# Performance work log

Hardware: AMD Instinct MI355X
Metric: run time of the kernel (lower is better)

Reference implementation:

```python
import jax, jax.numpy as jnp
import numpy as np

B = 256
H = W = 14
HW = H * W
TS = 0.03  # sigmoid temperature
TC = 0.07  # contrastive temperature
TP_K = int(HW * 0.1)   # 19
TN_K = int(HW * 0.5)   # 98
EPS_NORM = 1e-12
EPS_PD = 1e-6  # torch F.pairwise_distance eps


def _l2norm(x, axis):
    n = jnp.sqrt(jnp.sum(x * x, axis=axis, keepdims=True))
    return x / jnp.maximum(n, EPS_NORM)


def _conv(x, w):
    return jax.lax.conv_general_dilated(
        x, w, window_strides=(1, 1), padding='SAME',
        dimension_numbers=('NCHW', 'OIHW', 'NCHW'))


def setup_inputs() -> dict:
    key = jax.random.key(0)
    ks = jax.random.split(key, 7)
    ev = jax.random.normal(ks[0], (B, 384, H, W), dtype=jnp.float32)
    ea = jax.random.normal(ks[1], (B, 2048), dtype=jnp.float32)
    masks = jax.random.randint(ks[2], (B, H, W), 0, 2).astype(jnp.int32)
    masks = masks.at[:, 0, 0].set(1)  # guarantee nonzero mask area
    W_fc1 = jax.random.normal(ks[3], (512, 2048), dtype=jnp.float32) * 0.02
    W_fc2 = jax.random.normal(ks[4], (512, 512), dtype=jnp.float32) * 0.02
    W_conv1 = jax.random.normal(ks[5], (512, 384, 3, 3), dtype=jnp.float32) * 0.02
    W_conv2 = jax.random.normal(ks[6], (512, 512, 3, 3), dtype=jnp.float32) * 0.02
    return {'ev': ev, 'ea': ea, 'masks': masks, 'W_fc1': W_fc1,
            'W_fc2': W_fc2, 'W_conv1': W_conv1, 'W_conv2': W_conv2}


def reference(ev, ea, masks, W_fc1, W_fc2, W_conv1, W_conv2):
    # Audio_Proj: fc2(relu(fc1(ea)))  -> (B, 512)
    fa = jnp.maximum(ea @ W_fc1.T, 0.0) @ W_fc2.T

    # Visual_Proj: conv2(relu(conv1(ev))) -> (B, 512, 14, 14)
    fv_map = _conv(jnp.maximum(_conv(ev, W_conv1), 0.0), W_conv2)
    fv_map_norm = _l2norm(fv_map, axis=1)

    # masked mean pooling over the Ncut mask -> indicator vector (B, 512)
    m = masks.astype(jnp.float32)
    ind_vec = jnp.sum(fv_map * m[:, None], axis=(2, 3)) / jnp.sum(m, axis=(1, 2))[:, None]
    ind_vec_norm = _l2norm(ind_vec, axis=1)

    # Sij[i, j, p] = <fv_map_norm[i, :, p], ind_vec_norm[j]>  -> (B, B, HW)
    Sij = jnp.einsum('ichw,jc->ijhw', fv_map_norm, ind_vec_norm).reshape(B, B, HW)

    # per-row topk thresholds (kth largest / kth smallest)
    pos_thr = jax.lax.top_k(Sij, TP_K)[0][..., -1:]           # (B, B, 1)
    neg_thr = -jax.lax.top_k(-Sij, TN_K)[0][..., -1:]         # (B, B, 1)

    m_p = jax.nn.sigmoid((Sij - pos_thr) / TS)
    m_n = 1.0 - jax.nn.sigmoid((Sij - neg_thr) / TS)

    SP = jnp.sum(Sij * m_p, axis=-1) / jnp.sum(m_p, axis=-1)  # (B, B)
    SN = jnp.sum(Sij * m_n, axis=-1) / jnp.sum(m_n, axis=-1)  # (B, B)

    logits1 = jnp.concatenate([SP, SN], axis=1) / TC          # (B, 2B)
    logits2 = jnp.concatenate([SP.T, SN.T], axis=1) / TC
    labels = jnp.arange(B)
    loss1 = -jnp.mean(jax.nn.log_softmax(logits1, axis=-1)[labels, labels])
    loss2 = -jnp.mean(jax.nn.log_softmax(logits2, axis=-1)[labels, labels])

    # squared pairwise distance between detached ind_vec and fa (torch eps in diff)
    diff = jax.lax.stop_gradient(ind_vec)[:, None, :] - fa[None, :, :] + EPS_PD
    dist_mat = jnp.sum(diff * diff, axis=-1)                  # (B, B)

    ivn_d = jax.lax.stop_gradient(ind_vec_norm)
    vv_logits = ivn_d @ ivn_d.T
    eye = jnp.eye(B, dtype=jnp.float32)
    w = -vv_logits * (1.0 - eye) + eye
    dist_mat = dist_mat * w

    mask_mat = eye - (1.0 - eye) / (B - 1)
    loss3 = jnp.mean(jnp.maximum(jnp.sum(dist_mat * mask_mat, axis=1) + 0.6, 0.0))
    loss4 = jnp.mean(jnp.maximum(jnp.sum(dist_mat * mask_mat, axis=0) + 0.6, 0.0))

    return ((loss1 + loss2) / 2.0, (loss3 + loss4) / 2.0)
```

## Files before the change

### kernel.cpp

```cpp
#include <hip/hip_runtime.h>
#include <stdint.h>


typedef __attribute__((ext_vector_type(8))) short bf16x8;
typedef __attribute__((ext_vector_type(4))) short short4v;
typedef __attribute__((ext_vector_type(4))) float f32x4;

__device__ __forceinline__ unsigned short f2bf(float x) {
  unsigned u = __float_as_uint(x);
  unsigned r = u + 0x7FFFu + ((u >> 16) & 1u);
  return (unsigned short)(r >> 16);
}
__device__ __forceinline__ float bf2f(unsigned short h) {
  return __uint_as_float(((unsigned)h) << 16);
}

typedef const __attribute__((address_space(1))) void* gptr1_t;
typedef __attribute__((address_space(3))) void* lptr3_t;
__device__ __forceinline__ void gload_lds16(const void* g, void* l) {
  __builtin_amdgcn_global_load_lds((gptr1_t)g, (lptr3_t)l, 16, 0, 0);
}

__device__ __forceinline__ float waveSum(float v) {
#pragma unroll
  for (int m = 1; m < 64; m <<= 1) v += __shfl_xor(v, m, 64);
  return v;
}
__device__ __forceinline__ float waveMax(float v) {
#pragma unroll
  for (int m = 1; m < 64; m <<= 1) v = fmaxf(v, __shfl_xor(v, m, 64));
  return v;
}
template <int NW>
__device__ __forceinline__ float blockSum(float v) {
  __shared__ float sh[NW];
  v = waveSum(v);
  int wv = threadIdx.x >> 6, ln = threadIdx.x & 63;
  if (ln == 0) sh[wv] = v;
  __syncthreads();
  float r = 0.f;
#pragma unroll
  for (int w = 0; w < NW; ++w) r += sh[w];
  __syncthreads();
  return r;
}
template <int NW>
__device__ __forceinline__ float blockMax(float v) {
  __shared__ float sh[NW];
  v = waveMax(v);
  int wv = threadIdx.x >> 6, ln = threadIdx.x & 63;
  if (ln == 0) sh[wv] = v;
  __syncthreads();
  float r = -3.4e38f;
#pragma unroll
  for (int w = 0; w < NW; ++w) r = fmaxf(r, sh[w]);
  __syncthreads();
  return r;
}

#define RA 65536

template <int KC, int EPI>
__global__ __launch_bounds__(256, 2) void convtap6_k(
    const unsigned short* __restrict__ A, const unsigned short* __restrict__ Bw,
    unsigned short* __restrict__ C) {
  __shared__ __align__(16) short Ah[256 * 72];
  const int tid = threadIdx.x;
  const int wave = tid >> 6, lane = tid & 63;
  const int wm = wave >> 1, wn = wave & 1;
  const int quad = lane >> 4, tq = lane & 15;
  const int img = blockIdx.x, n0 = blockIdx.y * 128;

  int pab[7];
  {
    const int dh = tq >> 3;
    int wq = wm * 8 + (tq & 7);
    if (wq == 0) wq = 8;
    else if (wq == 15) wq = 7;
#pragma unroll
    for (int mi = 0; mi < 7; ++mi) {
      int pr = (1 + 2 * mi + dh) * 16 + wq;
      pab[mi] = (pr - 17) * 144 + quad * 16;
    }
  }
  const int gb = (n0 >> 4) + wn * 4;

  const char* Ab = (const char*)A;
  const char* AhB = (const char*)Ah;
  const int l16 = lane * 16;

  f32x4 acc[7][4];
#pragma unroll
  for (int mi = 0; mi < 7; ++mi)
#pragma unroll
    for (int ni = 0; ni < 4; ++ni) {
      f32x4 z = {0.f, 0.f, 0.f, 0.f};
      acc[mi][ni] = z;
    }

  auto stageA = [&](int kc) {
    size_t s0 = ((size_t)kc * RA + img * 256) * 144;
#pragma unroll
    for (int i = 0; i < 9; ++i) {
      int c = wave + i * 4;
      gload_lds16(Ab + s0 + (size_t)c * 1024 + l16, (char*)Ah + c * 1024);
    }
  };

  stageA(0);
  bf16x8 b0[4], b1[4];
  {
    const size_t w0 = ((size_t)gb * 128 + lane) * 8;
#pragma unroll
    for (int ni = 0; ni < 4; ++ni)
      b0[ni] = *(const bf16x8*)&Bw[w0 + (size_t)ni * 1024];
  }
  __syncthreads();

#pragma unroll 1
  for (int kc = 0; kc < KC; ++kc) {
    const size_t bk = ((size_t)kc * 4096 + gb * 128 + lane) * 8;
#pragma unroll
    for (int t = 0; t < 9; ++t) {
      const size_t tof = (size_t)t * KC * 32768;
#pragma unroll
      for (int ni = 0; ni < 4; ++ni)
        b1[ni] = *(const bf16x8*)&Bw[bk + tof + (size_t)ni * 1024 + 512];
      bf16x8 b0n[4];
      const bool last = (t == 8) && (kc == KC - 1);
      if (!last) {
        const size_t nbase =
            (t < 8) ? bk + (size_t)(t + 1) * KC * 32768 : bk + 32768;
#pragma unroll
        for (int ni = 0; ni < 4; ++ni)
          b0n[ni] = *(const bf16x8*)&Bw[nbase + (size_t)ni * 1024];
      }
      const int OFF = (17 + (t / 3 - 1) * 16 + (t % 3 - 1)) * 144;
      bf16x8 af0[7], af1[7];
#pragma unroll
      for (int mi = 0; mi < 7; ++mi)
        af0[mi] = *(const bf16x8*)(AhB + pab[mi] + OFF);
#pragma unroll
      for (int mi = 0; mi < 7; ++mi)
        af1[mi] = *(const bf16x8*)(AhB + pab[mi] + OFF + 64);
      __builtin_amdgcn_s_setprio(1);
#pragma unroll
      for (int mi = 0; mi < 7; ++mi)
#pragma unroll
        for (int ni = 0; ni < 4; ++ni)
          acc[mi][ni] = __builtin_amdgcn_mfma_f32_16x16x32_bf16(
              af0[mi], b0[ni], acc[mi][ni], 0, 0, 0);
#pragma unroll
      for (int mi = 0; mi < 7; ++mi)
#pragma unroll
        for (int ni = 0; ni < 4; ++ni)
          acc[mi][ni] = __builtin_amdgcn_mfma_f32_16x16x32_bf16(
              af1[mi], b1[ni], acc[mi][ni], 0, 0, 0);
      __builtin_amdgcn_s_setprio(0);
      if (!last) {
#pragma unroll
        for (int ni = 0; ni < 4; ++ni) b0[ni] = b0n[ni];
      }
    }
    if (kc + 1 < KC) {
      __syncthreads();
      stageA(kc + 1);
      __syncthreads();
    }
  }

#pragma unroll
  for (int mi = 0; mi < 7; ++mi) {
#pragma unroll
    for (int r = 0; r < 4; ++r) {
      int idx = quad * 4 + r;
      int wv = wm * 8 + (idx & 7);
      if (wv == 0 || wv == 15) continue;
      int hh = 1 + 2 * mi + (idx >> 3);
      short4v s4;
#pragma unroll
      for (int ni = 0; ni < 4; ++ni) {
        float v = acc[mi][ni][r];
        s4[ni] = (short)f2bf(EPI == 0 ? fmaxf(v, 0.f) : v);
      }
      if (EPI == 0) {
        int cell = img * 256 + hh * 16 + wv;
        int slice = (n0 >> 6) + wn;
        size_t ob = ((size_t)slice * RA + cell) * 72 + tq * 4;
        *(short4v*)&C[ob] = s4;
      } else {
        int p = (hh - 1) * 14 + (wv - 1);
        size_t ob = (size_t)(img * 196 + p) * 512 + n0 + wn * 64 + tq * 4;
        *(short4v*)&C[ob] = s4;
      }
    }
  }
}

template <int K, int NLD, int EPI>
__global__ __launch_bounds__(256, 2) void gemm1_k(
    const unsigned short* __restrict__ A, const unsigned short* __restrict__ Bw,
    void* __restrict__ C, const float* __restrict__ rs) {
  __shared__ short As[128 * 64];
  __shared__ short Bs[128 * 64];
  const int tid = threadIdx.x;
  const int wave = tid >> 6, lane = tid & 63;
  const int m0 = blockIdx.x * 128, n0 = blockIdx.y * 128;
  const int rr8 = lane >> 3, seg = lane & 7, gseg = seg ^ rr8;
  const int wm = wave >> 1, wn = wave & 1;
  const int quad = lane >> 4, tq = lane & 15;

  size_t asrc[4], bsrc[4];
#pragma unroll
  for (int i8 = 0; i8 < 4; ++i8) {
    int rloc = wave * 32 + i8 * 8 + rr8;
    asrc[i8] = (size_t)(m0 + rloc) * K + gseg * 8;
    bsrc[i8] = (size_t)(n0 + rloc) * K + gseg * 8;
  }

  f32x4 acc[4][4];
#pragma unroll
  for (int mi = 0; mi < 4; ++mi)
#pragma unroll
    for (int ni = 0; ni < 4; ++ni) {
      f32x4 z = {0.f, 0.f, 0.f, 0.f};
      acc[mi][ni] = z;
    }

#pragma unroll 1
  for (int kc2 = 0; kc2 < K / 64; ++kc2) {
    int kb = kc2 * 64;
    __syncthreads();
#pragma unroll
    for (int i8 = 0; i8 < 4; ++i8) {
      gload_lds16(A + asrc[i8] + kb, &As[(wave * 32 + i8 * 8) * 64]);
      gload_lds16(Bw + bsrc[i8] + kb, &Bs[(wave * 32 + i8 * 8) * 64]);
    }
    __syncthreads();
#pragma unroll
    for (int h = 0; h < 2; ++h) {
      bf16x8 af[4], bfr[4];
#pragma unroll
      for (int mi = 0; mi < 4; ++mi) {
        int row = wm * 64 + mi * 16 + tq;
        af[mi] = *(const bf16x8*)&As[row * 64 +
                                     ((((h << 2) | quad) ^ (row & 7)) << 3)];
      }
#pragma unroll
      for (int ni = 0; ni < 4; ++ni) {
        int row = wn * 64 + ni * 16 + tq;
        bfr[ni] = *(const bf16x8*)&Bs[row * 64 +
                                      ((((h << 2) | quad) ^ (row & 7)) << 3)];
      }
#pragma unroll
      for (int mi = 0; mi < 4; ++mi)
#pragma unroll
        for (int ni = 0; ni < 4; ++ni)
          acc[mi][ni] = __builtin_amdgcn_mfma_f32_16x16x32_bf16(
              af[mi], bfr[ni], acc[mi][ni], 0, 0, 0);
    }
  }

#pragma unroll
  for (int mi = 0; mi < 4; ++mi) {
#pragma unroll
    for (int r = 0; r < 4; ++r) {
      int m = m0 + wm * 64 + mi * 16 + quad * 4 + r;
      float sc = (EPI == 3) ? rs[m] : 1.f;
      size_t obase = (size_t)m * NLD + n0 + wn * 64 + tq;
#pragma unroll
      for (int ni = 0; ni < 4; ++ni) {
        float v = acc[mi][ni][r];
        size_t idx = obase + ni * 16;
        if (EPI == 0)
          ((unsigned short*)C)[idx] = f2bf(fmaxf(v, 0.f));
        else if (EPI == 2)
          ((float*)C)[idx] = v;
        else
          ((float*)C)[idx] = v * sc;
      }
    }
  }
}

__global__ __launch_bounds__(256, 2) void gemm_xv_k(
    const unsigned short* __restrict__ ivpb, const unsigned short* __restrict__ fab,
    const unsigned short* __restrict__ indnb, float* __restrict__ Xm,
    float* __restrict__ Vm) {
  const unsigned short* A = blockIdx.z ? indnb : ivpb;
  const unsigned short* Bw = blockIdx.z ? indnb : fab;
  float* C = blockIdx.z ? Vm : Xm;
  __shared__ short As[128 * 64];
  __shared__ short Bs[128 * 64];
  const int tid = threadIdx.x;
  const int wave = tid >> 6, lane = tid & 63;
  const int m0 = blockIdx.x * 128, n0 = blockIdx.y * 128;
  const int rr8 = lane >> 3, seg = lane & 7, gseg = seg ^ rr8;
  const int wm = wave >> 1, wn = wave & 1;
  const int quad = lane >> 4, tq = lane & 15;
  size_t asrc[4], bsrc[4];
#pragma unroll
  for (int i8 = 0; i8 < 4; ++i8) {
    int rloc = wave * 32 + i8 * 8 + rr8;
    asrc[i8] = (size_t)(m0 + rloc) * 512 + gseg * 8;
    bsrc[i8] = (size_t)(n0 + rloc) * 512 + gseg * 8;
  }
  f32x4 acc[4][4];
#pragma unroll
  for (int mi = 0; mi < 4; ++mi)
#pragma unroll
    for (int ni = 0; ni < 4; ++ni) {
      f32x4 z = {0.f, 0.f, 0.f, 0.f};
      acc[mi][ni] = z;
    }
#pragma unroll 1
  for (int kc2 = 0; kc2 < 8; ++kc2) {
    int kb = kc2 * 64;
    __syncthreads();
#pragma unroll
    for (int i8 = 0; i8 < 4; ++i8) {
      gload_lds16(A + asrc[i8] + kb, &As[(wave * 32 + i8 * 8) * 64]);
      gload_lds16(Bw + bsrc[i8] + kb, &Bs[(wave * 32 + i8 * 8) * 64]);
    }
    __syncthreads();
#pragma unroll
    for (int h = 0; h < 2; ++h) {
      bf16x8 af[4], bfr[4];
#pragma unroll
      for (int mi = 0; mi < 4; ++mi) {
        int row = wm * 64 + mi * 16 + tq;
        af[mi] = *(const bf16x8*)&As[row * 64 +
                                     ((((h << 2) | quad) ^ (row & 7)) << 3)];
      }
#pragma unroll
      for (int ni = 0; ni < 4; ++ni) {
        int row = wn * 64 + ni * 16 + tq;
        bfr[ni] = *(const bf16x8*)&Bs[row * 64 +
                                      ((((h << 2) | quad) ^ (row & 7)) << 3)];
      }
#pragma unroll
      for (int mi = 0; mi < 4; ++mi)
#pragma unroll
        for (int ni = 0; ni < 4; ++ni)
          acc[mi][ni] = __builtin_amdgcn_mfma_f32_16x16x32_bf16(
              af[mi], bfr[ni], acc[mi][ni], 0, 0, 0);
    }
  }
#pragma unroll
  for (int mi = 0; mi < 4; ++mi)
#pragma unroll
    for (int r = 0; r < 4; ++r) {
      int m = m0 + wm * 64 + mi * 16 + quad * 4 + r;
      size_t obase = (size_t)m * 256 + n0 + wn * 64 + tq;
#pragma unroll
      for (int ni = 0; ni < 4; ++ni) C[obase + ni * 16] = acc[mi][ni][r];
    }
}

__global__ void prep_all_k(const float* __restrict__ ea,
                           const float* __restrict__ Wf1,
                           const float* __restrict__ Wf2,
                           const float* __restrict__ Wc1,
                           const float* __restrict__ Wc2,
                           unsigned short* __restrict__ eab,
                           unsigned short* __restrict__ wf1b,
                           unsigned short* __restrict__ wf2b,
                           unsigned short* __restrict__ wb1,
                           unsigned short* __restrict__ wb2,
                           unsigned int* __restrict__ x1u) {
  int i = blockIdx.x * 256 + threadIdx.x;
  if (i < 524288) {
    eab[i] = f2bf(ea[i]);
  } else if (i < 1572864) {
    int j = i - 524288;
    wf1b[j] = f2bf(Wf1[j]);
  } else if (i < 1835008) {
    int j = i - 1572864;
    wf2b[j] = f2bf(Wf2[j]);
  } else if (i < 3604480) {
    int j = i - 1835008;
    int t = j / (6 * 32768), r = j - t * (6 * 32768);
    int kc = r / 32768, r2 = r - kc * 32768;
    int g = r2 >> 10, h = (r2 >> 9) & 1, quad = (r2 >> 7) & 3;
    int tq = (r2 >> 3) & 15, jj = r2 & 7;
    int n = g * 16 + tq, cin = kc * 64 + h * 32 + quad * 8 + jj;
    wb1[j] = f2bf(Wc1[(n * 384 + cin) * 9 + t]);
  } else if (i < 5963776) {
    int j = i - 3604480;
    int t = j / (8 * 32768), r = j - t * (8 * 32768);
    int kc = r / 32768, r2 = r - kc * 32768;
    int g = r2 >> 10, h = (r2 >> 9) & 1, quad = (r2 >> 7) & 3;
    int tq = (r2 >> 3) & 15, jj = r2 & 7;
    int n = g * 16 + tq;
    int cin = kc * 64 + (jj & 3) * 16 + h * 8 + quad * 2 + (jj >> 2);
    wb2[j] = f2bf(Wc2[(n * 512 + cin) * 9 + t]);
  } else {
    int j = i - 5963776;
    int hr = j >> 8, u = j & 255;
    int slice = u >> 5, uu = u & 31;
    int b = hr / 60, c = hr - b * 60;
    int cell;
    if (c < 16) cell = c;
    else if (c < 32) cell = 240 + (c - 16);
    else if (c < 46) cell = (c - 31) * 16;
    else cell = (c - 45) * 16 + 15;
    x1u[((size_t)slice * RA + b * 256 + cell) * 36 + uu] = 0u;
  }
}

__global__ __launch_bounds__(256) void evpad_k(const float* __restrict__ ev,
                                               unsigned short* __restrict__ out) {
  int b = blockIdx.x, ct = blockIdx.y;
  __shared__ float tile[64][197];
  int tid = threadIdx.x;
  const float* src = ev + ((size_t)b * 384 + ct * 64) * 196;
#pragma unroll 1
  for (int it = 0; it < 49; ++it) {
    int idx = it * 256 + tid;
    int c = idx / 196, p = idx - c * 196;
    tile[c][p] = src[idx];
  }
  __syncthreads();
  unsigned short* dst = out + ((size_t)ct * RA + b * 256) * 72;
#pragma unroll 1
  for (int it = 0; it < 64; ++it) {
    int idx = it * 256 + tid;
    int cell = idx >> 6, c = idx & 63;
    int h = (cell >> 4) - 1, w = (cell & 15) - 1;
    float v = ((unsigned)h < 14u && (unsigned)w < 14u) ? tile[c][h * 14 + w]
                                                       : 0.f;
    dst[(size_t)cell * 72 + c] = f2bf(v);
  }
}


__global__ __launch_bounds__(512) void pool_k(
    const unsigned short* __restrict__ fv, const int* __restrict__ masks,
    unsigned short* __restrict__ indnb, unsigned short* __restrict__ ivpb,
    float* __restrict__ Pi, float* __restrict__ rn) {
  int b = blockIdx.x;
  int w = threadIdx.x >> 6, lane = threadIdx.x & 63;
  __shared__ float red[8][512];
  __shared__ float msh[8];
  float acc[8] = {0.f, 0.f, 0.f, 0.f, 0.f, 0.f, 0.f, 0.f};
  float msum = 0.f;
  for (int p = w; p < 196; p += 8) {
    float m = (float)masks[b * 196 + p];
    msum += m;
    uint4 d = *(const uint4*)(fv + (size_t)(b * 196 + p) * 512 + lane * 8);
    const unsigned short* hp = (const unsigned short*)&d;
    float ss = 0.f;
#pragma unroll
    for (int k = 0; k < 8; ++k) {
      float x = bf2f(hp[k]);
      ss += x * x;
      acc[k] += m * x;
    }
    ss = waveSum(ss);
    if (lane == 0) rn[b * 196 + p] = 1.f / fmaxf(sqrtf(ss), 1e-12f);
  }
#pragma unroll
  for (int k = 0; k < 8; ++k) red[w][lane * 8 + k] = acc[k];
  if (lane == 0) msh[w] = msum;
  __syncthreads();
  int tid = threadIdx.x;
  float s = 0.f, mtot = 0.f;
#pragma unroll
  for (int ww = 0; ww < 8; ++ww) {
    s += red[ww][tid];
    mtot += msh[ww];
  }
  float v = s / mtot;
  float ss2 = blockSum<8>(v * v);
  float sc = 1.f / fmaxf(sqrtf(ss2), 1e-12f);
  indnb[b * 512 + tid] = f2bf(v * sc);
  float ve = v + 1e-6f;
  ivpb[b * 512 + tid] = f2bf(ve);
  float p2 = blockSum<8>(ve * ve);
  if (tid == 0) Pi[b] = p2;
}

__global__ __launch_bounds__(512) void fanorm_k(const float* __restrict__ fa,
                                                unsigned short* __restrict__ fab,
                                                float* __restrict__ Qj) {
  int b = blockIdx.x, tid = threadIdx.x;
  int s64 = tid & 63;
  int chan = (tid & ~63) | ((s64 & 3) * 16 + (s64 >> 2));
  float v = fa[b * 512 + chan];
  fab[b * 512 + tid] = f2bf(v);
  float q = blockSum<8>(v * v);
  if (tid == 0) Qj[b] = q;
}


__device__ __forceinline__ float radix_kth(unsigned k0, unsigned k1, unsigned k2,
                                           unsigned k3, int k) {
  unsigned prefix = 0;
  int kk = k;
#pragma unroll 1
  for (int bit = 31; bit >= 14; --bit) {
    unsigned thi = (prefix >> bit) | 1u;
    int c = __popcll(__ballot((k0 >> bit) == thi)) +
            __popcll(__ballot((k1 >> bit) == thi)) +
            __popcll(__ballot((k2 >> bit) == thi)) +
            __popcll(__ballot((k3 >> bit) == thi));
    if (kk <= c)
      prefix |= (1u << bit);
    else
      kk -= c;
  }
  unsigned u = (prefix & 0x80000000u) ? (prefix ^ 0x80000000u) : ~prefix;
  return __uint_as_float(u);
}
__device__ __forceinline__ unsigned sortkey(float x) {
  unsigned u = __float_as_uint(x);
  return u ^ (((int)u >> 31) | 0x80000000u);
}

__global__ __launch_bounds__(256) void spsn_k(const float* __restrict__ Sij,
                                              float* __restrict__ SP,
                                              float* __restrict__ SN) {
  int i = blockIdx.x, jg = blockIdx.y;
  int tid = threadIdx.x, wave = tid >> 6, lane = tid & 63;
  __shared__ float tile[196 * 65];
#pragma unroll 1
  for (int it = 0; it < 49; ++it) {
    int lin = it * 256 + tid;
    int p = lin >> 6, j = lin & 63;
    tile[p * 65 + j] = Sij[(size_t)(i * 196 + p) * 256 + jg * 64 + j];
  }
  __syncthreads();
#pragma unroll 1
  for (int jj = 0; jj < 16; ++jj) {
    int j = jj * 4 + wave;
    float v0 = tile[lane * 65 + j];
    float v1 = tile[(lane + 64) * 65 + j];
    float v2 = tile[(lane + 128) * 65 + j];
    bool val3 = lane < 4;
    float v3 = val3 ? tile[(lane + 192) * 65 + j] : 0.f;
    unsigned k0 = sortkey(v0), k1 = sortkey(v1), k2 = sortkey(v2);
    unsigned k3 = val3 ? sortkey(v3) : 0u;
    float thrP = radix_kth(k0, k1, k2, k3, 19);
    float thrN = radix_kth(k0, k1, k2, k3, 99);
    float spn = 0.f, spd = 0.f, snn = 0.f, snd = 0.f;
    const float invTS = 1.f / 0.03f;
#pragma unroll
    for (int q = 0; q < 4; ++q) {
      float v = (q == 0) ? v0 : (q == 1) ? v1 : (q == 2) ? v2 : v3;
      bool ok = (q < 3) || val3;
      if (ok) {
        float mp = 1.f / (1.f + __expf((thrP - v) * invTS));
        float mn = 1.f / (1.f + __expf((v - thrN) * invTS));
        spn += v * mp;
        spd += mp;
        snn += v * mn;
        snd += mn;
      }
    }
    spn = waveSum(spn); spd = waveSum(spd);
    snn = waveSum(snn); snd = waveSum(snd);
    if (lane == 0) {
      SP[i * 256 + jg * 64 + j] = spn / spd;
      SN[i * 256 + jg * 64 + j] = snn / snd;
    }
  }
}

__global__ __launch_bounds__(256) void loss12_k(const float* __restrict__ SP,
                                                const float* __restrict__ SN,
                                                float* __restrict__ out) {
  int r = blockIdx.x;
  int i = r & 255;
  bool col = r >= 256;
  int tid = threadIdx.x;
  const float invTC = 1.f / 0.07f;
  float a = (col ? SP[tid * 256 + i] : SP[i * 256 + tid]) * invTC;
  float b = (col ? SN[tid * 256 + i] : SN[i * 256 + tid]) * invTC;
  float mx = blockMax<4>(fmaxf(a, b));
  float se = blockSum<4>(__expf(a - mx) + __expf(b - mx));
  float lse = mx + __logf(se);
  if (tid == 0) {
    float diag = SP[i * 256 + i] * invTC;
    atomicAdd(out, -(diag - lse) * (1.f / 512.f));
  }
}

__global__ __launch_bounds__(256) void distcomb_k(
    const float* __restrict__ Pi, const float* __restrict__ Qj,
    const float* __restrict__ X, const float* __restrict__ V,
    float* __restrict__ val, float* __restrict__ out) {
  int i = blockIdx.x, j = threadIdx.x;
  float d = Pi[i] - 2.f * X[i * 256 + j] + Qj[j];
  float w = (i == j) ? 1.f : -V[i * 256 + j];
  float x = d * w;
  val[i * 256 + j] = x;
  __shared__ float diag_sh;
  if (j == i) diag_sh = x;
  float tot = blockSum<4>(x);
  if (j == 0) {
    float rs = diag_sh - (tot - diag_sh) * (1.f / 255.f);
    atomicAdd(out + 1, fmaxf(rs + 0.6f, 0.f) * (1.f / 512.f));
  }
}

__global__ __launch_bounds__(256) void loss4_k(const float* __restrict__ val,
                                               float* __restrict__ out) {
  int j = blockIdx.x, i = threadIdx.x;
  float x = val[i * 256 + j];
  __shared__ float diag_sh;
  if (i == j) diag_sh = x;
  float tot = blockSum<4>(x);
  if (i == 0) {
    float cs = diag_sh - (tot - diag_sh) * (1.f / 255.f);
    atomicAdd(out + 1, fmaxf(cs + 0.6f, 0.f) * (1.f / 512.f));
  }
}


extern "C" void kernel_launch(void* const* d_in, const int* in_sizes, int n_in,
                              void* d_out, int out_size, void* d_ws,
                              size_t ws_size, hipStream_t stream) {
  (void)in_sizes; (void)n_in; (void)out_size; (void)ws_size;
  const float* ev = (const float*)d_in[0];
  const float* ea = (const float*)d_in[1];
  const int* msk = (const int*)d_in[2];
  const float* Wf1 = (const float*)d_in[3];
  const float* Wf2 = (const float*)d_in[4];
  const float* Wc1 = (const float*)d_in[5];
  const float* Wc2 = (const float*)d_in[6];
  float* out = (float*)d_out;
  char* ws = (char*)d_ws;

  size_t off = 0;
  auto alloc = [&](size_t bytes) {
    void* p = ws + off;
    off = (off + bytes + 255) & ~(size_t)255;
    return p;
  };
  unsigned short* evb = (unsigned short*)alloc((size_t)6 * RA * 144);
  unsigned short* fv = evb;
  unsigned short* x1b = (unsigned short*)alloc((size_t)8 * RA * 144);
  float* Sij = (float*)x1b;
  unsigned short* wb1 = (unsigned short*)alloc((size_t)9 * 6 * 32768 * 2);
  unsigned short* wb2 = (unsigned short*)alloc((size_t)9 * 8 * 32768 * 2);
  unsigned short* eab = (unsigned short*)alloc((size_t)256 * 2048 * 2);
  unsigned short* wf1b = (unsigned short*)alloc((size_t)512 * 2048 * 2);
  unsigned short* wf2b = (unsigned short*)alloc((size_t)512 * 512 * 2);
  unsigned short* hb = (unsigned short*)alloc((size_t)256 * 512 * 2);
  float* fa = (float*)alloc((size_t)256 * 512 * 4);
  unsigned short* indnb = (unsigned short*)alloc((size_t)256 * 512 * 2);
  unsigned short* ivpb = (unsigned short*)alloc((size_t)256 * 512 * 2);
  unsigned short* fab = (unsigned short*)alloc((size_t)256 * 512 * 2);
  float* Pi = (float*)alloc(256 * 4);
  float* Qj = (float*)alloc(256 * 4);
  float* Xm = (float*)alloc((size_t)256 * 256 * 4);
  float* Vm = (float*)alloc((size_t)256 * 256 * 4);
  float* rn = (float*)alloc((size_t)50176 * 4);
  float* SP = (float*)alloc((size_t)256 * 256 * 4);
  float* SN = (float*)alloc((size_t)256 * 256 * 4);
  float* val = (float*)alloc((size_t)256 * 256 * 4);

  hipMemsetAsync(out, 0, 2 * sizeof(float), stream);

  prep_all_k<<<38656, 256, 0, stream>>>(ea, Wf1, Wf2, Wc1, Wc2, eab, wf1b,
                                        wf2b, wb1, wb2, (unsigned int*)x1b);
  evpad_k<<<dim3(256, 6), 256, 0, stream>>>(ev, evb);

  convtap6_k<6, 0><<<dim3(256, 4), 256, 0, stream>>>(evb, wb1, x1b);
  gemm1_k<2048, 512, 0><<<dim3(2, 4), 256, 0, stream>>>(eab, wf1b, hb, nullptr);
  gemm1_k<512, 512, 2><<<dim3(2, 4), 256, 0, stream>>>(hb, wf2b, fa, nullptr);
  convtap6_k<8, 1><<<dim3(256, 4), 256, 0, stream>>>(x1b, wb2, fv);

  pool_k<<<256, 512, 0, stream>>>(fv, msk, indnb, ivpb, Pi, rn);
  fanorm_k<<<256, 512, 0, stream>>>(fa, fab, Qj);

  gemm1_k<512, 256, 3><<<dim3(392, 2), 256, 0, stream>>>(fv, indnb, Sij, rn);
  gemm_xv_k<<<dim3(2, 2, 2), 256, 0, stream>>>(ivpb, fab, indnb, Xm, Vm);

  spsn_k<<<dim3(256, 4), 256, 0, stream>>>(Sij, SP, SN);
  loss12_k<<<512, 256, 0, stream>>>(SP, SN, out);
  distcomb_k<<<256, 256, 0, stream>>>(Pi, Qj, Xm, Vm, val, out);
  loss4_k<<<256, 256, 0, stream>>>(val, out);
}
```

Before: 777.4 us.

## Double-buffer GEMM LDS staging and merge small pool/fa and loss kernels

The two generic GEMM kernels now use two LDS buffers, so the global-to-LDS load of the next K-chunk is issued before the MFMA work on the current chunk, and there is one barrier per iteration instead of two. Separately, pool and fa-normalization are fused into one launch, and the loss12 and distcomb kernels are merged into one launch, to cut launch overhead. Doubling LDS to 64KB per block may reduce occupancy under the launch bound of 2 blocks per CU.

After: 767.8 us, median of 2. About the same (-1.2%).

```diff
diff --git a/kernel.cpp b/kernel.cpp
--- a/kernel.cpp
+++ b/kernel.cpp
@@ -201,8 +201,8 @@
 __global__ __launch_bounds__(256, 2) void gemm1_k(
     const unsigned short* __restrict__ A, const unsigned short* __restrict__ Bw,
     void* __restrict__ C, const float* __restrict__ rs) {
-  __shared__ short As[128 * 64];
-  __shared__ short Bs[128 * 64];
+  __shared__ short As[2][128 * 64];
+  __shared__ short Bs[2][128 * 64];
   const int tid = threadIdx.x;
   const int wave = tid >> 6, lane = tid & 63;
   const int m0 = blockIdx.x * 128, n0 = blockIdx.y * 128;
@@ -218,6 +218,15 @@
     bsrc[i8] = (size_t)(n0 + rloc) * K + gseg * 8;
   }
 
+  auto stage = [&](int kc2, int buf) {
+    int kb = kc2 * 64;
+#pragma unroll
+    for (int i8 = 0; i8 < 4; ++i8) {
+      gload_lds16(A + asrc[i8] + kb, &As[buf][(wave * 32 + i8 * 8) * 64]);
+      gload_lds16(Bw + bsrc[i8] + kb, &Bs[buf][(wave * 32 + i8 * 8) * 64]);
+    }
+  };
+
   f32x4 acc[4][4];
 #pragma unroll
   for (int mi = 0; mi < 4; ++mi)
@@ -227,30 +236,27 @@
       acc[mi][ni] = z;
     }
 
-#pragma unroll 1
-  for (int kc2 = 0; kc2 < K / 64; ++kc2) {
-    int kb = kc2 * 64;
-    __syncthreads();
-#pragma unroll
-    for (int i8 = 0; i8 < 4; ++i8) {
-      gload_lds16(A + asrc[i8] + kb, &As[(wave * 32 + i8 * 8) * 64]);
-      gload_lds16(Bw + bsrc[i8] + kb, &Bs[(wave * 32 + i8 * 8) * 64]);
-    }
-    __syncthreads();
+  const int NK = K / 64;
+  stage(0, 0);
+  __syncthreads();
+#pragma unroll 1
+  for (int kc2 = 0; kc2 < NK; ++kc2) {
+    const int cur = kc2 & 1;
+    if (kc2 + 1 < NK) stage(kc2 + 1, cur ^ 1);
 #pragma unroll
     for (int h = 0; h < 2; ++h) {
       bf16x8 af[4], bfr[4];
 #pragma unroll
       for (int mi = 0; mi < 4; ++mi) {
         int row = wm * 64 + mi * 16 + tq;
-        af[mi] = *(const bf16x8*)&As[row * 64 +
-                                     ((((h << 2) | quad) ^ (row & 7)) << 3)];
+        af[mi] = *(const bf16x8*)&As[cur][row * 64 +
+                                         ((((h << 2) | quad) ^ (row & 7)) << 3)];
       }
 #pragma unroll
       for (int ni = 0; ni < 4; ++ni) {
         int row = wn * 64 + ni * 16 + tq;
-        bfr[ni] = *(const bf16x8*)&Bs[row * 64 +
-                                      ((((h << 2) | quad) ^ (row & 7)) << 3)];
+        bfr[ni] = *(const bf16x8*)&Bs[cur][row * 64 +
+                                           ((((h << 2) | quad) ^ (row & 7)) << 3)];
       }
 #pragma unroll
       for (int mi = 0; mi < 4; ++mi)
@@ -259,6 +265,7 @@
           acc[mi][ni] = __builtin_amdgcn_mfma_f32_16x16x32_bf16(
               af[mi], bfr[ni], acc[mi][ni], 0, 0, 0);
     }
+    __syncthreads();
   }
 
 #pragma unroll
@@ -290,8 +297,8 @@
   const unsigned short* A = blockIdx.z ? indnb : ivpb;
   const unsigned short* Bw = blockIdx.z ? indnb : fab;
   float* C = blockIdx.z ? Vm : Xm;
-  __shared__ short As[128 * 64];
-  __shared__ short Bs[128 * 64];
+  __shared__ short As[2][128 * 64];
+  __shared__ short Bs[2][128 * 64];
   const int tid = threadIdx.x;
   const int wave = tid >> 6, lane = tid & 63;
   const int m0 = blockIdx.x * 128, n0 = blockIdx.y * 128;
@@ -305,6 +312,14 @@
     asrc[i8] = (size_t)(m0 + rloc) * 512 + gseg * 8;
     bsrc[i8] = (size_t)(n0 + rloc) * 512 + gseg * 8;
   }
+  auto stage = [&](int kc2, int buf) {
+    int kb = kc2 * 64;
+#pragma unroll
+    for (int i8 = 0; i8 < 4; ++i8) {
+      gload_lds16(A + asrc[i8] + kb, &As[buf][(wave * 32 + i8 * 8) * 64]);
+      gload_lds16(Bw + bsrc[i8] + kb, &Bs[buf][(wave * 32 + i8 * 8) * 64]);
+    }
+  };
   f32x4 acc[4][4];
 #pragma unroll
   for (int mi = 0; mi < 4; ++mi)
@@ -313,30 +328,26 @@
       f32x4 z = {0.f, 0.f, 0.f, 0.f};
       acc[mi][ni] = z;
     }
+  stage(0, 0);
+  __syncthreads();
 #pragma unroll 1
   for (int kc2 = 0; kc2 < 8; ++kc2) {
-    int kb = kc2 * 64;
-    __syncthreads();
-#pragma unroll
-    for (int i8 = 0; i8 < 4; ++i8) {
-      gload_lds16(A + asrc[i8] + kb, &As[(wave * 32 + i8 * 8) * 64]);
-      gload_lds16(Bw + bsrc[i8] + kb, &Bs[(wave * 32 + i8 * 8) * 64]);
-    }
-    __syncthreads();
+    const int cur = kc2 & 1;
+    if (kc2 + 1 < 8) stage(kc2 + 1, cur ^ 1);
 #pragma unroll
     for (int h = 0; h < 2; ++h) {
       bf16x8 af[4], bfr[4];
 #pragma unroll
       for (int mi = 0; mi < 4; ++mi) {
         int row = wm * 64 + mi * 16 + tq;
-        af[mi] = *(const bf16x8*)&As[row * 64 +
-                                     ((((h << 2) | quad) ^ (row & 7)) << 3)];
+        af[mi] = *(const bf16x8*)&As[cur][row * 64 +
+                                         ((((h << 2) | quad) ^ (row & 7)) << 3)];
       }
 #pragma unroll
       for (int ni = 0; ni < 4; ++ni) {
         int row = wn * 64 + ni * 16 + tq;
-        bfr[ni] = *(const bf16x8*)&Bs[row * 64 +
-                                      ((((h << 2) | quad) ^ (row & 7)) << 3)];
+        bfr[ni] = *(const bf16x8*)&Bs[cur][row * 64 +
+                                           ((((h << 2) | quad) ^ (row & 7)) << 3)];
       }
 #pragma unroll
       for (int mi = 0; mi < 4; ++mi)
@@ -345,6 +356,7 @@
           acc[mi][ni] = __builtin_amdgcn_mfma_f32_16x16x32_bf16(
               af[mi], bfr[ni], acc[mi][ni], 0, 0, 0);
     }
+    __syncthreads();
   }
 #pragma unroll
   for (int mi = 0; mi < 4; ++mi)
@@ -433,13 +445,25 @@
   }
 }
 
-
-__global__ __launch_bounds__(512) void pool_k(
+__global__ __launch_bounds__(512) void poolfa_k(
     const unsigned short* __restrict__ fv, const int* __restrict__ masks,
-    unsigned short* __restrict__ indnb, unsigned short* __restrict__ ivpb,
-    float* __restrict__ Pi, float* __restrict__ rn) {
-  int b = blockIdx.x;
-  int w = threadIdx.x >> 6, lane = threadIdx.x & 63;
+    const float* __restrict__ fa, unsigned short* __restrict__ indnb,
+    unsigned short* __restrict__ ivpb, unsigned short* __restrict__ fab,
+    float* __restrict__ Pi, float* __restrict__ Qj, float* __restrict__ rn) {
+  int bid = blockIdx.x;
+  int tid = threadIdx.x;
+  if (bid >= 256) {
+    int b = bid - 256;
+    int s64 = tid & 63;
+    int chan = (tid & ~63) | ((s64 & 3) * 16 + (s64 >> 2));
+    float v = fa[b * 512 + chan];
+    fab[b * 512 + tid] = f2bf(v);
+    float q = blockSum<8>(v * v);
+    if (tid == 0) Qj[b] = q;
+    return;
+  }
+  int b = bid;
+  int w = tid >> 6, lane = tid & 63;
   __shared__ float red[8][512];
   __shared__ float msh[8];
   float acc[8] = {0.f, 0.f, 0.f, 0.f, 0.f, 0.f, 0.f, 0.f};
@@ -463,7 +487,6 @@
   for (int k = 0; k < 8; ++k) red[w][lane * 8 + k] = acc[k];
   if (lane == 0) msh[w] = msum;
   __syncthreads();
-  int tid = threadIdx.x;
   float s = 0.f, mtot = 0.f;
 #pragma unroll
   for (int ww = 0; ww < 8; ++ww) {
@@ -478,18 +501,6 @@
   ivpb[b * 512 + tid] = f2bf(ve);
   float p2 = blockSum<8>(ve * ve);
   if (tid == 0) Pi[b] = p2;
-}
-
-__global__ __launch_bounds__(512) void fanorm_k(const float* __restrict__ fa,
-                                                unsigned short* __restrict__ fab,
-                                                float* __restrict__ Qj) {
-  int b = blockIdx.x, tid = threadIdx.x;
-  int s64 = tid & 63;
-  int chan = (tid & ~63) | ((s64 & 3) * 16 + (s64 >> 2));
-  float v = fa[b * 512 + chan];
-  fab[b * 512 + tid] = f2bf(v);
-  float q = blockSum<8>(v * v);
-  if (tid == 0) Qj[b] = q;
 }
 
 
@@ -566,40 +577,39 @@
   }
 }
 
-__global__ __launch_bounds__(256) void loss12_k(const float* __restrict__ SP,
-                                                const float* __restrict__ SN,
-                                                float* __restrict__ out) {
-  int r = blockIdx.x;
-  int i = r & 255;
-  bool col = r >= 256;
-  int tid = threadIdx.x;
-  const float invTC = 1.f / 0.07f;
-  float a = (col ? SP[tid * 256 + i] : SP[i * 256 + tid]) * invTC;
-  float b = (col ? SN[tid * 256 + i] : SN[i * 256 + tid]) * invTC;
-  float mx = blockMax<4>(fmaxf(a, b));
-  float se = blockSum<4>(__expf(a - mx) + __expf(b - mx));
-  float lse = mx + __logf(se);
-  if (tid == 0) {
-    float diag = SP[i * 256 + i] * invTC;
-    atomicAdd(out, -(diag - lse) * (1.f / 512.f));
-  }
-}
-
-__global__ __launch_bounds__(256) void distcomb_k(
+__global__ __launch_bounds__(256) void lossA_k(
+    const float* __restrict__ SP, const float* __restrict__ SN,
     const float* __restrict__ Pi, const float* __restrict__ Qj,
     const float* __restrict__ X, const float* __restrict__ V,
     float* __restrict__ val, float* __restrict__ out) {
-  int i = blockIdx.x, j = threadIdx.x;
-  float d = Pi[i] - 2.f * X[i * 256 + j] + Qj[j];
-  float w = (i == j) ? 1.f : -V[i * 256 + j];
-  float x = d * w;
-  val[i * 256 + j] = x;
-  __shared__ float diag_sh;
-  if (j == i) diag_sh = x;
-  float tot = blockSum<4>(x);
-  if (j == 0) {
-    float rs = diag_sh - (tot - diag_sh) * (1.f / 255.f);
-    atomicAdd(out + 1, fmaxf(rs + 0.6f, 0.f) * (1.f / 512.f));
+  int r = blockIdx.x;
+  int tid = threadIdx.x;
+  if (r < 512) {
+    int i = r & 255;
+    bool col = r >= 256;
+    const float invTC = 1.f / 0.07f;
+    float a = (col ? SP[tid * 256 + i] : SP[i * 256 + tid]) * invTC;
+    float b = (col ? SN[tid * 256 + i] : SN[i * 256 + tid]) * invTC;
+    float mx = blockMax<4>(fmaxf(a, b));
+    float se = blockSum<4>(__expf(a - mx) + __expf(b - mx));
+    float lse = mx + __logf(se);
+    if (tid == 0) {
+      float diag = SP[i * 256 + i] * invTC;
+      atomicAdd(out, -(diag - lse) * (1.f / 512.f));
+    }
+  } else {
+    int i = r - 512, j = tid;
+    float d = Pi[i] - 2.f * X[i * 256 + j] + Qj[j];
+    float w = (i == j) ? 1.f : -V[i * 256 + j];
+    float x = d * w;
+    val[i * 256 + j] = x;
+    __shared__ float diag_sh;
+    if (j == i) diag_sh = x;
+    float tot = blockSum<4>(x);
+    if (j == 0) {
+      float rs = diag_sh - (tot - diag_sh) * (1.f / 255.f);
+      atomicAdd(out + 1, fmaxf(rs + 0.6f, 0.f) * (1.f / 512.f));
+    }
   }
 }
 
@@ -671,14 +681,12 @@
   gemm1_k<512, 512, 2><<<dim3(2, 4), 256, 0, stream>>>(hb, wf2b, fa, nullptr);
   convtap6_k<8, 1><<<dim3(256, 4), 256, 0, stream>>>(x1b, wb2, fv);
 
-  pool_k<<<256, 512, 0, stream>>>(fv, msk, indnb, ivpb, Pi, rn);
-  fanorm_k<<<256, 512, 0, stream>>>(fa, fab, Qj);
+  poolfa_k<<<512, 512, 0, stream>>>(fv, msk, fa, indnb, ivpb, fab, Pi, Qj, rn);
 
   gemm1_k<512, 256, 3><<<dim3(392, 2), 256, 0, stream>>>(fv, indnb, Sij, rn);
   gemm_xv_k<<<dim3(2, 2, 2), 256, 0, stream>>>(ivpb, fab, indnb, Xm, Vm);
 
   spsn_k<<<dim3(256, 4), 256, 0, stream>>>(Sij, SP, SN);
-  loss12_k<<<512, 256, 0, stream>>>(SP, SN, out);
-  distcomb_k<<<256, 256, 0, stream>>>(Pi, Qj, Xm, Vm, val, out);
+  lossA_k<<<768, 256, 0, stream>>>(SP, SN, Pi, Qj, Xm, Vm, val, out);
   loss4_k<<<256, 256, 0, stream>>>(val, out);
 }
```
